# Optimization experiments

Measured on AMD Instinct MI355X. Metric: run time of the kernel, lower is better.

Reference implementation:

```python
import jax, jax.numpy as jnp
import numpy as np

NUM_HEADS = 8
NUM_POINTS = 4


def setup_inputs() -> dict:
    key = jax.random.key(0)
    ks = jax.random.split(key, 8)
    B, N, C, H, W = 8, 8192, 256, 128, 128
    HP2 = NUM_HEADS * NUM_POINTS * 2
    HP = NUM_HEADS * NUM_POINTS
    query = jax.random.normal(ks[0], (B, N, C), jnp.float32)
    reference_points = jax.random.uniform(ks[1], (B, N, 2), dtype=jnp.float32)
    value = jax.random.normal(ks[2], (B, C, H, W), jnp.float32)
    # learned params (offset gen is zero-init in the original; use small random
    W_off = jax.random.normal(ks[3], (C, HP2), jnp.float32) * 0.02
    b_off = jnp.zeros((HP2,), jnp.float32)
    W_attn = jax.random.normal(ks[4], (C, HP), jnp.float32) * (1.0 / np.sqrt(C))
    b_attn = jnp.zeros((HP,), jnp.float32)
    W_out = jax.random.normal(ks[5], (C, C), jnp.float32) * (1.0 / np.sqrt(C))
    b_out = jnp.zeros((C,), jnp.float32)
    return dict(query=query, reference_points=reference_points, value=value,
                W_off=W_off, b_off=b_off, W_attn=W_attn, b_attn=b_attn,
                W_out=W_out, b_out=b_out, H=H, W=W)


def reference(query, reference_points, value, W_off, b_off, W_attn, b_attn,
              W_out, b_out, H, W):
    B, N, C = query.shape
    Hh, P = NUM_HEADS, NUM_POINTS
    D = C // Hh

    offset = (query @ W_off + b_off).reshape(B, N, Hh, P, 2)
    attn = jax.nn.softmax((query @ W_attn + b_attn).reshape(B, N, Hh, P), axis=-1)

    # sampling locations in grid_sample convention: (x, y) in [-1, 1]
    ref = reference_points * 2.0 - 1.0
    loc = ref[:, :, None, None, :] + offset  # (B, N, Hh, P, 2)

    # value -> (B, Hh, H*W, D)
    val = value.reshape(B, Hh, D, H, W).transpose(0, 1, 3, 4, 2).reshape(B, Hh, H * W, D)

    # align_corners=False pixel coordinates
    x = (loc[..., 0] + 1.0) * (W * 0.5) - 0.5  # (B, N, Hh, P)
    y = (loc[..., 1] + 1.0) * (H * 0.5) - 0.5
    x0f = jnp.floor(x); y0f = jnp.floor(y)
    wx1 = x - x0f; wy1 = y - y0f
    x0 = x0f.astype(jnp.int32); y0 = y0f.astype(jnp.int32)
    x1 = x0 + 1; y1 = y0 + 1

    def gather(ix, iy, w):
        # bilinear corner gather with zero padding (mask out-of-bounds)
        valid = (ix >= 0) & (ix < W) & (iy >= 0) & (iy < H)
        idx = jnp.clip(iy, 0, H - 1) * W + jnp.clip(ix, 0, W - 1)  # (B,N,Hh,P)
        idx_t = idx.transpose(0, 2, 1, 3).reshape(B, Hh, N * P)
        g = jnp.take_along_axis(val, idx_t[..., None], axis=2)  # (B,Hh,N*P,D)
        g = g.reshape(B, Hh, N, P, D).transpose(0, 2, 1, 3, 4)  # (B,N,Hh,P,D)
        return g * (w * valid)[..., None]

    sampled = (gather(x0, y0, (1 - wx1) * (1 - wy1))
               + gather(x1, y0, wx1 * (1 - wy1))
               + gather(x0, y1, (1 - wx1) * wy1)
               + gather(x1, y1, wx1 * wy1))  # (B,N,Hh,P,D)

    out = jnp.einsum('bnhk,bnhkd->bnhd', attn, sampled).reshape(B, N, C)
    return out @ W_out + b_out
```

## Files before the change

### kernel.cpp

```cpp
#include <hip/hip_runtime.h>
#include <hip/hip_bf16.h>
#include <cstddef>

#define B_  8
#define N_  8192
#define C_  256
#define H_  128
#define W_  128
#define HH  8
#define PP  4
#define DD  32
#define HW  (H_ * W_)

typedef short bf16x8 __attribute__((ext_vector_type(8)));
typedef float f32x4  __attribute__((ext_vector_type(4)));

static __device__ __forceinline__ short f2bf_s(float f) {
    __hip_bfloat16 b = __float2bfloat16(f);
    return *reinterpret_cast<short*>(&b);
}
static __device__ __forceinline__ float bf_s2f(short s) {
    __hip_bfloat16 b = *reinterpret_cast<__hip_bfloat16*>(&s);
    return __bfloat162float(b);
}

__global__ __launch_bounds__(256) void kT(const float* __restrict__ value,
                                          __hip_bfloat16* __restrict__ val) {
    __shared__ float tile[32][65];
    const int bh   = blockIdx.y;
    const int pix0 = blockIdx.x * 64;
    const int t    = threadIdx.x;

    const float* src = value + (size_t)bh * 32 * HW + pix0;
#pragma unroll
    for (int i = 0; i < 8; ++i) {
        int d = i * 4 + (t >> 6);
        int p = t & 63;
        tile[d][p] = src[(size_t)d * HW + p];
    }
    __syncthreads();
    __hip_bfloat162* dst =
        (__hip_bfloat162*)(val + ((size_t)bh * HW + pix0) * 32);
#pragma unroll
    for (int j = 0; j < 4; ++j) {
        int p  = j * 16 + (t >> 4);
        int dd = (t & 15) * 2;
        __hip_bfloat162 pk;
        pk.x = __float2bfloat16(tile[dd][p]);
        pk.y = __float2bfloat16(tile[dd + 1][p]);
        dst[p * 16 + (t & 15)] = pk;
    }
}

__global__ __launch_bounds__(256) void kP(const float* __restrict__ W_off,
                                          const float* __restrict__ W_attn,
                                          short* __restrict__ Wc_hi,
                                          short* __restrict__ Wc_lo) {
    const int c = blockIdx.x;
    const int k = threadIdx.x;
    float v = (c < 64) ? W_off[(size_t)k * 64 + c]
                       : W_attn[(size_t)k * 32 + (c - 64)];
    short h = f2bf_s(v);
    short l = f2bf_s(v - bf_s2f(h));
    Wc_hi[(size_t)c * 256 + k] = h;
    Wc_lo[(size_t)c * 256 + k] = l;
}

__global__ __launch_bounds__(256) void kA1M(const float* __restrict__ query,
                                            const float* __restrict__ refp,
                                            const short* __restrict__ Wc_hi,
                                            const short* __restrict__ Wc_lo,
                                            const float* __restrict__ b_off,
                                            const float* __restrict__ b_attn,
                                            float4* __restrict__ locattn) {
    __shared__ __align__(16) char smem[57344];
    short* As_hi = (short*)smem;
    short* As_lo = (short*)(smem + 16384);
    short* Bs_hi = (short*)(smem + 32768);
    short* Bs_lo = (short*)(smem + 45056);
    float* Ct    = (float*)smem;

    const int t    = threadIdx.x;
    const int lane = t & 63;
    const int w    = t >> 6;
    const int wm   = (w & 1) * 64;
    const int wn   = (w >> 1) * 48;
    const int quad = lane >> 4;
    const int l16  = lane & 15;
    const int row0 = blockIdx.x * 128;

    f32x4 acc[4][3];
#pragma unroll
    for (int mt = 0; mt < 4; ++mt)
#pragma unroll
        for (int nt = 0; nt < 3; ++nt)
            acc[mt][nt] = (f32x4){0.f, 0.f, 0.f, 0.f};

    for (int k0c = 0; k0c < 4; ++k0c) {
#pragma unroll
        for (int i = 0; i < 8; ++i) {
            int f   = t + i * 256;
            int row = f >> 4;
            int kq4 = f & 15;
            float4 q = *(const float4*)&query[(size_t)(row0 + row) * 256 +
                                              k0c * 64 + kq4 * 4];
            short4 hv, lv;
            hv.x = f2bf_s(q.x); lv.x = f2bf_s(q.x - bf_s2f(hv.x));
            hv.y = f2bf_s(q.y); lv.y = f2bf_s(q.y - bf_s2f(hv.y));
            hv.z = f2bf_s(q.z); lv.z = f2bf_s(q.z - bf_s2f(hv.z));
            hv.w = f2bf_s(q.w); lv.w = f2bf_s(q.w - bf_s2f(hv.w));
            int base = row * 64 + (((kq4 >> 1) ^ (row & 7)) * 8) + (kq4 & 1) * 4;
            *(short4*)&As_hi[base] = hv;
            *(short4*)&As_lo[base] = lv;
        }
#pragma unroll
        for (int i = 0; i < 3; ++i) {
            int idx = t + i * 256;
            int n   = idx >> 3;
            int kb  = idx & 7;
            int dst = n * 64 + ((kb ^ (n & 7)) * 8);
            *(uint4*)&Bs_hi[dst] =
                *(const uint4*)&Wc_hi[(size_t)n * 256 + k0c * 64 + kb * 8];
            *(uint4*)&Bs_lo[dst] =
                *(const uint4*)&Wc_lo[(size_t)n * 256 + k0c * 64 + kb * 8];
        }
        __syncthreads();

#pragma unroll
        for (int ks = 0; ks < 2; ++ks) {
            const int kq = ks * 4 + quad;
            bf16x8 ah[4], al[4], bh[3], bl[3];
#pragma unroll
            for (int mt = 0; mt < 4; ++mt) {
                int m = wm + mt * 16 + l16;
                ah[mt] = *(const bf16x8*)&As_hi[m * 64 + (kq ^ (m & 7)) * 8];
                al[mt] = *(const bf16x8*)&As_lo[m * 64 + (kq ^ (m & 7)) * 8];
            }
#pragma unroll
            for (int nt = 0; nt < 3; ++nt) {
                int n = wn + nt * 16 + l16;
                bh[nt] = *(const bf16x8*)&Bs_hi[n * 64 + (kq ^ (n & 7)) * 8];
                bl[nt] = *(const bf16x8*)&Bs_lo[n * 64 + (kq ^ (n & 7)) * 8];
            }
#pragma unroll
            for (int mt = 0; mt < 4; ++mt)
#pragma unroll
                for (int nt = 0; nt < 3; ++nt)
                    acc[mt][nt] = __builtin_amdgcn_mfma_f32_16x16x32_bf16(
                        ah[mt], bh[nt], acc[mt][nt], 0, 0, 0);
#pragma unroll
            for (int mt = 0; mt < 4; ++mt)
#pragma unroll
                for (int nt = 0; nt < 3; ++nt)
                    acc[mt][nt] = __builtin_amdgcn_mfma_f32_16x16x32_bf16(
                        ah[mt], bl[nt], acc[mt][nt], 0, 0, 0);
#pragma unroll
            for (int mt = 0; mt < 4; ++mt)
#pragma unroll
                for (int nt = 0; nt < 3; ++nt)
                    acc[mt][nt] = __builtin_amdgcn_mfma_f32_16x16x32_bf16(
                        al[mt], bh[nt], acc[mt][nt], 0, 0, 0);
        }
        __syncthreads();
    }

#pragma unroll
    for (int mt = 0; mt < 4; ++mt) {
#pragma unroll
        for (int nt = 0; nt < 3; ++nt) {
            int col = wn + nt * 16 + l16;
#pragma unroll
            for (int rI = 0; rI < 4; ++rI) {
                int row = wm + mt * 16 + quad * 4 + rI;
                Ct[row * 100 + col] = acc[mt][nt][rI];
            }
        }
    }
    __syncthreads();

    const int rg = t >> 3;
    const int h  = t & 7;
    float boff[8];
#pragma unroll
    for (int j = 0; j < 8; ++j) boff[j] = b_off[h * 8 + j];
    float batn[4];
#pragma unroll
    for (int j = 0; j < 4; ++j) batn[j] = b_attn[h * 4 + j];

#pragma unroll
    for (int r = 0; r < 4; ++r) {
        int row  = rg * 4 + r;
        int rowg = row0 + row;
        int bb   = rowg >> 13;
        int nn   = rowg & 8191;
        float rx = refp[(size_t)rowg * 2 + 0];
        float ry = refp[(size_t)rowg * 2 + 1];
        float4 lg4 = *(const float4*)&Ct[row * 100 + 64 + h * 4];
        float lg[4] = {lg4.x + batn[0], lg4.y + batn[1],
                       lg4.z + batn[2], lg4.w + batn[3]};
        float m = fmaxf(fmaxf(lg[0], lg[1]), fmaxf(lg[2], lg[3]));
        float e[4];
        float s = 0.f;
#pragma unroll
        for (int p = 0; p < 4; ++p) { e[p] = __expf(lg[p] - m); s += e[p]; }
        float inv = 1.f / s;
        float4 o0 = *(const float4*)&Ct[row * 100 + h * 8];
        float4 o1 = *(const float4*)&Ct[row * 100 + h * 8 + 4];
        float ox[4] = {o0.x + boff[0], o0.z + boff[2],
                       o1.x + boff[4], o1.z + boff[6]};
        float oy[4] = {o0.y + boff[1], o0.w + boff[3],
                       o1.y + boff[5], o1.w + boff[7]};
#pragma unroll
        for (int p = 0; p < 4; ++p) {
            float x = (rx * 2.f + ox[p]) * (W_ * 0.5f) - 0.5f;
            float y = (ry * 2.f + oy[p]) * (H_ * 0.5f) - 0.5f;
            locattn[(((size_t)bb * HH + h) * N_ + nn) * PP + p] =
                make_float4(x, y, e[p] * inv, 0.f);
        }
    }
}

__global__ __launch_bounds__(256) void kA2(const float4* __restrict__ locattn,
                                           const __hip_bfloat16* __restrict__ val,
                                           __hip_bfloat16* __restrict__ mid) {
    __shared__ float2 ow[64][4][4];

    const int t  = threadIdx.x;
    const int bh = blockIdx.y;
    const int b  = bh >> 3;
    const int h  = bh & 7;
    const int n0 = blockIdx.x * 64;

    {
        const int r = t >> 2;
        const int p = t & 3;
        float4 L = locattn[((size_t)bh * N_ + n0 + r) * PP + p];
        float x = L.x, y = L.y, a = L.z;
        float xf = floorf(x), yf = floorf(y);
        int x0 = (int)xf, y0 = (int)yf;
        int x1 = x0 + 1, y1 = y0 + 1;
        float wx1 = x - xf, wy1 = y - yf;
        float wx0 = 1.f - wx1, wy0 = 1.f - wy1;
        int cx0 = min(max(x0, 0), W_ - 1);
        int cx1 = min(max(x1, 0), W_ - 1);
        int cy0 = min(max(y0, 0), H_ - 1);
        int cy1 = min(max(y1, 0), H_ - 1);
        bool bx0 = (x0 >= 0) & (x0 < W_);
        bool bx1 = (x1 >= 0) & (x1 < W_);
        bool by0 = (y0 >= 0) & (y0 < H_);
        bool by1 = (y1 >= 0) & (y1 < H_);
        float w00 = a * wx0 * wy0 * ((bx0 & by0) ? 1.f : 0.f);
        float w10 = a * wx1 * wy0 * ((bx1 & by0) ? 1.f : 0.f);
        float w01 = a * wx0 * wy1 * ((bx0 & by1) ? 1.f : 0.f);
        float w11 = a * wx1 * wy1 * ((bx1 & by1) ? 1.f : 0.f);
        ow[r][p][0] = make_float2(__int_as_float(cy0 * W_ + cx0), w00);
        ow[r][p][1] = make_float2(__int_as_float(cy0 * W_ + cx1), w10);
        ow[r][p][2] = make_float2(__int_as_float(cy1 * W_ + cx0), w01);
        ow[r][p][3] = make_float2(__int_as_float(cy1 * W_ + cx1), w11);
    }
    __syncthreads();

    const int d  = t & 31;
    const int rg = t >> 5;
    const __hip_bfloat16* vb = val + (size_t)bh * HW * DD + d;
    __hip_bfloat16* mo = mid + ((size_t)b * N_ + n0) * C_ + h * DD + d;

#pragma unroll
    for (int j = 0; j < 8; ++j) {
        int r = rg * 8 + j;
        const float4* owp = (const float4*)&ow[r][0][0];
        float acc = 0.f;
#pragma unroll
        for (int p = 0; p < 4; ++p) {
            float4 u0 = owp[p * 2 + 0];
            float4 u1 = owp[p * 2 + 1];
            int o00 = __float_as_int(u0.x) * DD;
            int o10 = __float_as_int(u0.z) * DD;
            int o01 = __float_as_int(u1.x) * DD;
            int o11 = __float_as_int(u1.z) * DD;
            acc += u0.y * __bfloat162float(vb[o00]);
            acc += u0.w * __bfloat162float(vb[o10]);
            acc += u1.y * __bfloat162float(vb[o01]);
            acc += u1.w * __bfloat162float(vb[o11]);
        }
        mo[r * C_] = __float2bfloat16(acc);
    }
}

__global__ __launch_bounds__(256) void kW(const float* __restrict__ Wsrc,
                                          __hip_bfloat16* __restrict__ Wt) {
    __shared__ float tile[64][65];
    const int n0 = blockIdx.x * 64;
    const int k0 = blockIdx.y * 64;
    const int t  = threadIdx.x;
#pragma unroll
    for (int i = 0; i < 16; ++i) {
        int kk = i * 4 + (t >> 6);
        int nn = t & 63;
        tile[kk][nn] = Wsrc[(size_t)(k0 + kk) * 256 + n0 + nn];
    }
    __syncthreads();
#pragma unroll
    for (int i = 0; i < 16; ++i) {
        int nn = i * 4 + (t >> 6);
        int kk = t & 63;
        Wt[(size_t)(n0 + nn) * 256 + k0 + kk] = __float2bfloat16(tile[kk][nn]);
    }
}

__global__ __launch_bounds__(256) void kC(const short* __restrict__ mid,
                                          const short* __restrict__ Wt,
                                          const float* __restrict__ bias,
                                          float* __restrict__ out) {
    __shared__ __align__(16) short As[128 * 64];
    __shared__ __align__(16) short Bs[128 * 64];

    const int t    = threadIdx.x;
    const int lane = t & 63;
    const int w    = t >> 6;
    const int wm   = (w & 1) * 64;
    const int wn   = (w >> 1) * 64;
    const int row0 = blockIdx.x * 128;
    const int col0 = blockIdx.y * 128;

    f32x4 acc[4][4];
#pragma unroll
    for (int mt = 0; mt < 4; ++mt)
#pragma unroll
        for (int nt = 0; nt < 4; ++nt)
            acc[mt][nt] = (f32x4){0.f, 0.f, 0.f, 0.f};

    const int sr = t >> 3;
    const int kb = t & 7;

    for (int k0 = 0; k0 < 4; ++k0) {
#pragma unroll
        for (int i = 0; i < 4; ++i) {
            int row  = sr + i * 32;
            int kbs  = (kb ^ (row & 7)) * 8;
            *(uint4*)&As[row * 64 + kbs] =
                *(const uint4*)&mid[(size_t)(row0 + row) * 256 + k0 * 64 + kb * 8];
            *(uint4*)&Bs[row * 64 + kbs] =
                *(const uint4*)&Wt[(size_t)(col0 + row) * 256 + k0 * 64 + kb * 8];
        }
        __syncthreads();

#pragma unroll
        for (int ks = 0; ks < 2; ++ks) {
            const int kq = ks * 4 + (lane >> 4);
            bf16x8 af[4], bf[4];
#pragma unroll
            for (int mt = 0; mt < 4; ++mt) {
                int m = wm + mt * 16 + (lane & 15);
                af[mt] = *(const bf16x8*)&As[m * 64 + (kq ^ (m & 7)) * 8];
            }
#pragma unroll
            for (int nt = 0; nt < 4; ++nt) {
                int n = wn + nt * 16 + (lane & 15);
                bf[nt] = *(const bf16x8*)&Bs[n * 64 + (kq ^ (n & 7)) * 8];
            }
#pragma unroll
            for (int mt = 0; mt < 4; ++mt)
#pragma unroll
                for (int nt = 0; nt < 4; ++nt)
                    acc[mt][nt] = __builtin_amdgcn_mfma_f32_16x16x32_bf16(
                        af[mt], bf[nt], acc[mt][nt], 0, 0, 0);
        }
        __syncthreads();
    }

    const int cq = lane >> 4;
#pragma unroll
    for (int nt = 0; nt < 4; ++nt) {
        int col  = col0 + wn + nt * 16 + (lane & 15);
        float bv = bias[col];
#pragma unroll
        for (int mt = 0; mt < 4; ++mt) {
#pragma unroll
            for (int rI = 0; rI < 4; ++rI) {
                int rowg = row0 + wm + mt * 16 + cq * 4 + rI;
                out[(size_t)rowg * 256 + col] = acc[mt][nt][rI] + bv;
            }
        }
    }
}

extern "C" void kernel_launch(void* const* d_in, const int* in_sizes, int n_in,
                              void* d_out, int out_size, void* d_ws, size_t ws_size,
                              hipStream_t stream) {
    const float* query  = (const float*)d_in[0];
    const float* refp   = (const float*)d_in[1];
    const float* value  = (const float*)d_in[2];
    const float* W_off  = (const float*)d_in[3];
    const float* b_off  = (const float*)d_in[4];
    const float* W_attn = (const float*)d_in[5];
    const float* b_attn = (const float*)d_in[6];
    const float* W_out  = (const float*)d_in[7];
    const float* b_out  = (const float*)d_in[8];
    float* out = (float*)d_out;

    char*           ws      = (char*)d_ws;
    __hip_bfloat16* val     = (__hip_bfloat16*)(ws);
    float4*         locattn = (float4*)(ws + 67108864);
    __hip_bfloat16* mid     = (__hip_bfloat16*)(ws + 100663296);
    __hip_bfloat16* Wt      = (__hip_bfloat16*)(ws + 134217728);
    short*          Wc_hi   = (short*)(ws + 134348800);
    short*          Wc_lo   = (short*)(ws + 134397952);

    kT  <<<dim3(HW / 64, B_ * HH), 256, 0, stream>>>(value, val);
    kP  <<<dim3(96), 256, 0, stream>>>(W_off, W_attn, Wc_hi, Wc_lo);
    kW  <<<dim3(4, 4), 256, 0, stream>>>(W_out, Wt);
    kA1M<<<dim3((B_ * N_) / 128), 256, 0, stream>>>(query, refp, Wc_hi, Wc_lo,
                                                    b_off, b_attn, locattn);
    kA2 <<<dim3(N_ / 64, B_ * HH), 256, 0, stream>>>(locattn, val, mid);
    kC  <<<dim3((B_ * N_) / 128, C_ / 128), 256, 0, stream>>>(
        (const short*)mid, (const short*)Wt, b_out, out);
}
```

Measured before the change: 381.3 us.

## Widen value transpose tiles, merge weight prep kernels, store locattn row-major

The value transpose kernel now handles 256 pixels per block, reading with float4 loads and writing 16-byte bf16x8 vectors. The two small weight preparation kernels are merged into one launch, which removes one kernel launch. The sampling-location buffer is written in the natural row-major order of the projection GEMM, and the gather kernel's indexing is changed to match, so the GEMM epilogue stores become contiguous. The cost is more shared memory per transpose block and a strided float4 read pattern in kA2.

```diff
diff --git a/kernel.cpp b/kernel.cpp
--- a/kernel.cpp
+++ b/kernel.cpp
@@ -26,44 +26,68 @@
 
 __global__ __launch_bounds__(256) void kT(const float* __restrict__ value,
                                           __hip_bfloat16* __restrict__ val) {
-    __shared__ float tile[32][65];
+    __shared__ float tile[32][257];
     const int bh   = blockIdx.y;
-    const int pix0 = blockIdx.x * 64;
+    const int pix0 = blockIdx.x * 256;
     const int t    = threadIdx.x;
 
     const float* src = value + (size_t)bh * 32 * HW + pix0;
 #pragma unroll
     for (int i = 0; i < 8; ++i) {
-        int d = i * 4 + (t >> 6);
-        int p = t & 63;
-        tile[d][p] = src[(size_t)d * HW + p];
+        int d  = i * 4 + (t >> 6);
+        int p4 = t & 63;
+        float4 v = *(const float4*)&src[(size_t)d * HW + p4 * 4];
+        tile[d][p4 * 4 + 0] = v.x;
+        tile[d][p4 * 4 + 1] = v.y;
+        tile[d][p4 * 4 + 2] = v.z;
+        tile[d][p4 * 4 + 3] = v.w;
     }
     __syncthreads();
-    __hip_bfloat162* dst =
-        (__hip_bfloat162*)(val + ((size_t)bh * HW + pix0) * 32);
 #pragma unroll
     for (int j = 0; j < 4; ++j) {
-        int p  = j * 16 + (t >> 4);
-        int dd = (t & 15) * 2;
-        __hip_bfloat162 pk;
-        pk.x = __float2bfloat16(tile[dd][p]);
-        pk.y = __float2bfloat16(tile[dd + 1][p]);
-        dst[p * 16 + (t & 15)] = pk;
+        int pix = j * 64 + (t >> 2);
+        int d0  = (t & 3) * 8;
+        bf16x8 o;
+#pragma unroll
+        for (int k = 0; k < 8; ++k) o[k] = f2bf_s(tile[d0 + k][pix]);
+        *(bf16x8*)&val[((size_t)bh * HW + pix0 + pix) * 32 + d0] = o;
     }
 }
 
 __global__ __launch_bounds__(256) void kP(const float* __restrict__ W_off,
                                           const float* __restrict__ W_attn,
                                           short* __restrict__ Wc_hi,
-                                          short* __restrict__ Wc_lo) {
-    const int c = blockIdx.x;
-    const int k = threadIdx.x;
-    float v = (c < 64) ? W_off[(size_t)k * 64 + c]
-                       : W_attn[(size_t)k * 32 + (c - 64)];
-    short h = f2bf_s(v);
-    short l = f2bf_s(v - bf_s2f(h));
-    Wc_hi[(size_t)c * 256 + k] = h;
-    Wc_lo[(size_t)c * 256 + k] = l;
+                                          short* __restrict__ Wc_lo,
+                                          const float* __restrict__ Wsrc,
+                                          __hip_bfloat16* __restrict__ Wt) {
+    __shared__ float tile[64][65];
+    const int t = threadIdx.x;
+    if (blockIdx.x < 96) {
+        const int c = blockIdx.x;
+        float v = (c < 64) ? W_off[(size_t)t * 64 + c]
+                           : W_attn[(size_t)t * 32 + (c - 64)];
+        short h = f2bf_s(v);
+        short l = f2bf_s(v - bf_s2f(h));
+        Wc_hi[(size_t)c * 256 + t] = h;
+        Wc_lo[(size_t)c * 256 + t] = l;
+    } else {
+        const int bx = blockIdx.x - 96;
+        const int n0 = (bx & 3) * 64;
+        const int k0 = (bx >> 2) * 64;
+#pragma unroll
+        for (int i = 0; i < 16; ++i) {
+            int kk = i * 4 + (t >> 6);
+            int nn = t & 63;
+            tile[kk][nn] = Wsrc[(size_t)(k0 + kk) * 256 + n0 + nn];
+        }
+        __syncthreads();
+#pragma unroll
+        for (int i = 0; i < 16; ++i) {
+            int nn = i * 4 + (t >> 6);
+            int kk = t & 63;
+            Wt[(size_t)(n0 + nn) * 256 + k0 + kk] = __float2bfloat16(tile[kk][nn]);
+        }
+    }
 }
 
 __global__ __launch_bounds__(256) void kA1M(const float* __restrict__ query,
@@ -191,8 +215,6 @@
     for (int r = 0; r < 4; ++r) {
         int row  = rg * 4 + r;
         int rowg = row0 + row;
-        int bb   = rowg >> 13;
-        int nn   = rowg & 8191;
         float rx = refp[(size_t)rowg * 2 + 0];
         float ry = refp[(size_t)rowg * 2 + 1];
         float4 lg4 = *(const float4*)&Ct[row * 100 + 64 + h * 4];
@@ -214,7 +236,7 @@
         for (int p = 0; p < 4; ++p) {
             float x = (rx * 2.f + ox[p]) * (W_ * 0.5f) - 0.5f;
             float y = (ry * 2.f + oy[p]) * (H_ * 0.5f) - 0.5f;
-            locattn[(((size_t)bb * HH + h) * N_ + nn) * PP + p] =
+            locattn[(size_t)rowg * 32 + h * 4 + p] =
                 make_float4(x, y, e[p] * inv, 0.f);
         }
     }
@@ -234,7 +256,7 @@
     {
         const int r = t >> 2;
         const int p = t & 3;
-        float4 L = locattn[((size_t)bh * N_ + n0 + r) * PP + p];
+        float4 L = locattn[((size_t)b * N_ + n0 + r) * 32 + h * 4 + p];
         float x = L.x, y = L.y, a = L.z;
         float xf = floorf(x), yf = floorf(y);
         int x0 = (int)xf, y0 = (int)yf;
@@ -287,27 +309,6 @@
     }
 }
 
-__global__ __launch_bounds__(256) void kW(const float* __restrict__ Wsrc,
-                                          __hip_bfloat16* __restrict__ Wt) {
-    __shared__ float tile[64][65];
-    const int n0 = blockIdx.x * 64;
-    const int k0 = blockIdx.y * 64;
-    const int t  = threadIdx.x;
-#pragma unroll
-    for (int i = 0; i < 16; ++i) {
-        int kk = i * 4 + (t >> 6);
-        int nn = t & 63;
-        tile[kk][nn] = Wsrc[(size_t)(k0 + kk) * 256 + n0 + nn];
-    }
-    __syncthreads();
-#pragma unroll
-    for (int i = 0; i < 16; ++i) {
-        int nn = i * 4 + (t >> 6);
-        int kk = t & 63;
-        Wt[(size_t)(n0 + nn) * 256 + k0 + kk] = __float2bfloat16(tile[kk][nn]);
-    }
-}
-
 __global__ __launch_bounds__(256) void kC(const short* __restrict__ mid,
                                           const short* __restrict__ Wt,
                                           const float* __restrict__ bias,
@@ -407,9 +408,8 @@
     short*          Wc_hi   = (short*)(ws + 134348800);
     short*          Wc_lo   = (short*)(ws + 134397952);
 
-    kT  <<<dim3(HW / 64, B_ * HH), 256, 0, stream>>>(value, val);
-    kP  <<<dim3(96), 256, 0, stream>>>(W_off, W_attn, Wc_hi, Wc_lo);
-    kW  <<<dim3(4, 4), 256, 0, stream>>>(W_out, Wt);
+    kT  <<<dim3(HW / 256, B_ * HH), 256, 0, stream>>>(value, val);
+    kP  <<<dim3(112), 256, 0, stream>>>(W_off, W_attn, Wc_hi, Wc_lo, W_out, Wt);
     kA1M<<<dim3((B_ * N_) / 128), 256, 0, stream>>>(query, refp, Wc_hi, Wc_lo,
                                                     b_off, b_attn, locattn);
     kA2 <<<dim3(N_ / 64, B_ * HH), 256, 0, stream>>>(locattn, val, mid);
```

After: 383.4 us. No clear change (+0.5%).
